# Optimization experiments

Hardware: AMD Instinct MI355X
Metric: run time of the kernel (lower is better)

## Reference

```python
import jax, jax.numpy as jnp
import numpy as np

B, S, H, NH, HD, L, I, M = 2, 2048, 768, 12, 64, 6, 3072, 256
VOCAB, TYPES = 30522, 2
EPS = 1e-6  # layernorm epsilon and FAVOR+ numerical stabilizer


def layer_norm(x, g, b):
    mu = jnp.mean(x, axis=-1, keepdims=True)
    var = jnp.mean(jax.lax.square(x), axis=-1, keepdims=True) - jax.lax.square(mu)
    return (x - mu) * jax.lax.rsqrt(var + EPS) * g + b


def favor_attention(q, k, v, mask, proj):
    # q,k,v: [B,S,NH,HD]; proj: [M,HD] random features; mask: [B,S] float
    dn = 1.0 / np.sqrt(np.sqrt(HD))      # data normalizer for softmax kernel
    ratio = 1.0 / np.sqrt(M)
    qn, kn = q * dn, k * dn
    qp = jnp.einsum('bsnd,md->bsnm', qn, proj)
    kp = jnp.einsum('bsnd,md->bsnm', kn, proj)
    qd = 0.5 * jnp.sum(qn * qn, axis=-1, keepdims=True)
    kd = 0.5 * jnp.sum(kn * kn, axis=-1, keepdims=True)
    # stabilizers: per-position max for queries, global (seq+feature) max for keys
    q_prime = ratio * (jnp.exp(qp - qd - jnp.max(qp, axis=-1, keepdims=True)) + EPS)
    k_prime = ratio * (jnp.exp(kp - kd - jnp.max(kp, axis=(1, 3), keepdims=True)) + EPS)
    k_prime = k_prime * mask[:, :, None, None]
    kv = jnp.einsum('bsnm,bsnd->bnmd', k_prime, v)          # [B,NH,M,HD]
    num = jnp.einsum('bsnm,bnmd->bsnd', q_prime, kv)        # [B,S,NH,HD]
    den = jnp.einsum('bsnm,bnm->bsn', q_prime, jnp.sum(k_prime, axis=1))
    return num / den[..., None]


def setup_inputs() -> dict:
    key = jax.random.key(0)
    ks = jax.random.split(key, 32)
    f = lambda i, shape, s=0.02: (jax.random.normal(ks[i], shape, jnp.float32) * s)
    inp = {
        'input_ids': jax.random.randint(ks[0], (B, S), 0, VOCAB, jnp.int32),
        'token_type_ids': jax.random.randint(ks[1], (B, S), 0, TYPES, jnp.int32),
        'position_ids': jnp.tile(jnp.arange(S, dtype=jnp.int32)[None, :], (B, 1)),
        'attention_mask': jnp.ones((B, S), jnp.int32),
        'word_emb': f(2, (VOCAB, H), 0.1),
        'pos_emb': f(3, (S, H), 0.1),
        'type_emb': f(4, (TYPES, H), 0.1),
        'emb_ln_g': jnp.ones((H,), jnp.float32),
        'emb_ln_b': jnp.zeros((H,), jnp.float32),
        'wq': f(5, (L, H, NH, HD)), 'bq': jnp.zeros((L, NH, HD), jnp.float32),
        'wk': f(6, (L, H, NH, HD)), 'bk': jnp.zeros((L, NH, HD), jnp.float32),
        'wv': f(7, (L, H, NH, HD)), 'bv': jnp.zeros((L, NH, HD), jnp.float32),
        'wo': f(8, (L, NH, HD, H)), 'bo': jnp.zeros((L, H), jnp.float32),
        'ln1_g': jnp.ones((L, H), jnp.float32), 'ln1_b': jnp.zeros((L, H), jnp.float32),
        'wi': f(9, (L, H, I)), 'bi': jnp.zeros((L, I), jnp.float32),
        'wo2': f(10, (L, I, H)), 'bo2': jnp.zeros((L, H), jnp.float32),
        'ln2_g': jnp.ones((L, H), jnp.float32), 'ln2_b': jnp.zeros((L, H), jnp.float32),
        'proj': jax.random.normal(ks[11], (L, M, HD), jnp.float32),
    }
    return inp


def reference(input_ids, token_type_ids, position_ids, attention_mask,
              word_emb, pos_emb, type_emb, emb_ln_g, emb_ln_b,
              wq, bq, wk, bk, wv, bv, wo, bo, ln1_g, ln1_b,
              wi, bi, wo2, bo2, ln2_g, ln2_b, proj):
    mask = attention_mask.astype(jnp.float32)
    x = word_emb[input_ids] + pos_emb[position_ids] + type_emb[token_type_ids]
    x = layer_norm(x, emb_ln_g, emb_ln_b)
    for l in range(L):
        q = jnp.einsum('bsh,hnd->bsnd', x, wq[l]) + bq[l]
        k = jnp.einsum('bsh,hnd->bsnd', x, wk[l]) + bk[l]
        v = jnp.einsum('bsh,hnd->bsnd', x, wv[l]) + bv[l]
        att = favor_attention(q, k, v, mask, proj[l])
        att = jnp.einsum('bsnd,ndh->bsh', att, wo[l]) + bo[l]
        a = layer_norm(att + x, ln1_g[l], ln1_b[l])
        inter = jax.nn.gelu(jnp.einsum('bsh,hi->bsi', a, wi[l]) + bi[l])
        out = jnp.einsum('bsi,ih->bsh', inter, wo2[l]) + bo2[l]
        x = layer_norm(out + a, ln2_g[l], ln2_b[l])
    return x
```

## Files before the change

### kernel.cpp

```cpp
#include <hip/hip_runtime.h>
#include <hip/hip_bf16.h>

#define B_ 2
#define S_ 2048
#define H_ 768
#define NH_ 12
#define HD_ 64
#define L_ 6
#define I_ 3072
#define M_ 256
#define BS_ 4096
#define R_ 49152
#define NXH_ 3145728
#define EPS_ 1e-6f
#define DN_ 0.35355339059327373f
#define RATIO_ 0.0625f

typedef __attribute__((ext_vector_type(8))) short bf16x8;
typedef __attribute__((ext_vector_type(4))) float f32x4;

__device__ __forceinline__ void gload16(const void* g, void* l) {
    __builtin_amdgcn_global_load_lds(
        (const __attribute__((address_space(1))) void*)g,
        (__attribute__((address_space(3))) void*)l, 16, 0, 0);
}

__device__ __forceinline__ float gelu_f(float x) {
    const float c = 0.7978845608028654f;
    float x3 = x * x * x;
    return 0.5f * x * (1.0f + tanhf(c * (x + 0.044715f * x3)));
}

__device__ __forceinline__ unsigned enc_f(float f) {
    unsigned u = __float_as_uint(f);
    return (u & 0x80000000u) ? ~u : (u | 0x80000000u);
}
__device__ __forceinline__ float dec_f(unsigned u) {
    return (u & 0x80000000u) ? __uint_as_float(u & 0x7fffffffu) : __uint_as_float(~u);
}

__device__ __forceinline__ void blockReduceSum2(float& a, float& b) {
    __shared__ float sa[4], sb[4];
    int lane = threadIdx.x & 63, wid = threadIdx.x >> 6;
    #pragma unroll
    for (int off = 32; off; off >>= 1) {
        a += __shfl_down(a, off, 64);
        b += __shfl_down(b, off, 64);
    }
    __syncthreads();
    if (lane == 0) { sa[wid] = a; sb[wid] = b; }
    __syncthreads();
    a = sa[0] + sa[1] + sa[2] + sa[3];
    b = sb[0] + sb[1] + sb[2] + sb[3];
    __syncthreads();
}

template<int ACT, int OUTMODE>
__global__ __launch_bounds__(256) void gemm_pipe3_kernel(
    const __hip_bfloat16* __restrict__ A, const __hip_bfloat16* __restrict__ BT,
    const float* __restrict__ bias, void* __restrict__ Cv,
    int K, int lda, int ldb, int ldc, float* __restrict__ aux)
{
    __shared__ __align__(16) unsigned short As[3][128][32];
    __shared__ __align__(16) unsigned short Bs[3][128][32];
    const int tid = threadIdx.x, lane = tid & 63, wid = tid >> 6;
    const int wr = wid >> 1, wc = wid & 1;
    const size_t r0 = (size_t)blockIdx.y * 128;
    const int n0 = blockIdx.x * 128;
    const size_t kbase = (size_t)blockIdx.z * (size_t)K;

    const int srow = lane >> 2;
    const int selem = ((lane & 3) ^ ((srow >> 1) & 3)) * 8;
    const unsigned short* ga0 = (const unsigned short*)A + (r0 + wid * 32 + srow) * (size_t)lda + kbase + selem;
    const unsigned short* gb0 = (const unsigned short*)BT + ((size_t)n0 + wid * 32 + srow) * (size_t)ldb + kbase + selem;

    f32x4 acc[4][4];
    #pragma unroll
    for (int i = 0; i < 4; i++)
        #pragma unroll
        for (int j = 0; j < 4; j++)
            acc[i][j] = (f32x4){0.f, 0.f, 0.f, 0.f};

    const int lr = lane & 15;
    const int rc8 = (((lane >> 4) ^ ((lr >> 1) & 3))) * 8;

#define STAGE_(t) { const int bb_ = (t) % 3; const int kk_ = (t) * 32;            \
    gload16(ga0 + kk_, &As[bb_][wid * 32][0]);                                    \
    gload16(ga0 + kk_ + 16 * (size_t)lda, &As[bb_][wid * 32 + 16][0]);            \
    gload16(gb0 + kk_, &Bs[bb_][wid * 32][0]);                                    \
    gload16(gb0 + kk_ + 16 * (size_t)ldb, &Bs[bb_][wid * 32 + 16][0]); }

#define ITER_(t, VMSTR, DOSTAGE) {                                                \
    if (DOSTAGE) STAGE_((t) + 2);                                                 \
    asm volatile("s_waitcnt vmcnt(" VMSTR ")" ::: "memory");                      \
    __builtin_amdgcn_sched_barrier(0);                                            \
    __builtin_amdgcn_s_barrier();                                                 \
    __builtin_amdgcn_sched_barrier(0);                                            \
    const int bb_ = (t) % 3;                                                      \
    bf16x8 af[4], bfv[4];                                                         \
    _Pragma("unroll") for (int i = 0; i < 4; i++)                                 \
        af[i] = *(const bf16x8*)&As[bb_][wr * 64 + i * 16 + lr][rc8];             \
    _Pragma("unroll") for (int j = 0; j < 4; j++)                                 \
        bfv[j] = *(const bf16x8*)&Bs[bb_][wc * 64 + j * 16 + lr][rc8];            \
    __builtin_amdgcn_s_setprio(1);                                                \
    _Pragma("unroll") for (int i = 0; i < 4; i++)                                 \
        _Pragma("unroll") for (int j = 0; j < 4; j++)                             \
            acc[i][j] = __builtin_amdgcn_mfma_f32_16x16x32_bf16(af[i], bfv[j], acc[i][j], 0, 0, 0); \
    __builtin_amdgcn_s_setprio(0);                                                \
    __builtin_amdgcn_s_barrier();                                                 \
    __builtin_amdgcn_sched_barrier(0); }

    const int nT = K >> 5;
    STAGE_(0); STAGE_(1);
    for (int t = 0; t < nT - 2; ++t) ITER_(t, "8", true);
    ITER_(nT - 2, "4", false);
    ITER_(nT - 1, "0", false);
#undef ITER_
#undef STAGE_

    const int rr = (lane >> 4) * 4;
    const int cc = lane & 15;
    if (OUTMODE == 3) {
        float* fpl = aux + (size_t)blockIdx.z * NXH_;
        #pragma unroll
        for (int i = 0; i < 4; i++) {
            #pragma unroll
            for (int j = 0; j < 4; j++) {
                size_t col = (size_t)n0 + wc * 64 + j * 16 + cc;
                #pragma unroll
                for (int rg = 0; rg < 4; rg++) {
                    size_t row = r0 + wr * 64 + i * 16 + rr + rg;
                    fpl[row * (size_t)ldc + col] = acc[i][j][rg];
                }
            }
        }
    } else if (OUTMODE == 1) {
        #pragma unroll
        for (int i = 0; i < 4; i++) {
            #pragma unroll
            for (int j = 0; j < 4; j++) {
                size_t col = (size_t)n0 + wc * 64 + j * 16 + cc;
                float bv_ = bias ? bias[col] : 0.f;
                #pragma unroll
                for (int rg = 0; rg < 4; rg++) {
                    size_t row = r0 + wr * 64 + i * 16 + rr + rg;
                    float v = acc[i][j][rg] + bv_;
                    if (ACT == 1) v = gelu_f(v);
                    ((__hip_bfloat16*)Cv)[row * (size_t)ldc + col] = __float2bfloat16(v);
                }
            }
        }
    } else {
        const size_t seg = (size_t)n0 / 768;
        const int colbase = n0 - (int)seg * 768;
        #pragma unroll
        for (int i = 0; i < 4; i++) {
            #pragma unroll
            for (int rg = 0; rg < 4; rg++) {
                size_t row = r0 + wr * 64 + i * 16 + rr + rg;
                float ss = 0.f;
                #pragma unroll
                for (int j = 0; j < 4; j++) {
                    int colw = wc * 64 + j * 16 + cc;
                    size_t col = (size_t)n0 + colw;
                    float bv_ = bias ? bias[col] : 0.f;
                    float v = acc[i][j][rg] + bv_;
                    __hip_bfloat16 hb = __float2bfloat16(v);
                    ((__hip_bfloat16*)Cv)[seg * (size_t)NXH_ + row * 768 + colbase + colw] = hb;
                    float vr = __bfloat162float(hb);
                    ss += vr * vr;
                }
                #pragma unroll
                for (int off = 1; off <= 8; off <<= 1)
                    ss += __shfl_xor(ss, off, 64);
                if (seg < 2 && (lane & 15) == 0) {
                    int nh = colbase / 64 + wc;
                    aux[seg * (size_t)R_ + row * 12 + nh] = 0.5f * DN_ * DN_ * ss;
                }
            }
        }
    }
}

__global__ __launch_bounds__(256) void gemm_pipe3_n64_kernel(
    const __hip_bfloat16* __restrict__ A, const __hip_bfloat16* __restrict__ BT,
    const float* __restrict__ bias, float* __restrict__ C,
    int K, int lda, int ldb, int ldc)
{
    __shared__ __align__(16) unsigned short As[3][128][32];
    __shared__ __align__(16) unsigned short Bs[3][64][32];
    const int tid = threadIdx.x, lane = tid & 63, wid = tid >> 6;
    const size_t r0 = (size_t)blockIdx.y * 128;
    const int n0 = blockIdx.x * 64;

    const int srow = lane >> 2;
    const int selem = ((lane & 3) ^ ((srow >> 1) & 3)) * 8;
    const unsigned short* ga0 = (const unsigned short*)A + (r0 + wid * 32 + srow) * (size_t)lda + selem;
    const unsigned short* gb0 = (const unsigned short*)BT + ((size_t)n0 + wid * 16 + srow) * (size_t)ldb + selem;

    f32x4 acc[2][4];
    #pragma unroll
    for (int i = 0; i < 2; i++)
        #pragma unroll
        for (int j = 0; j < 4; j++)
            acc[i][j] = (f32x4){0.f, 0.f, 0.f, 0.f};

    const int lr = lane & 15;
    const int rc8 = (((lane >> 4) ^ ((lr >> 1) & 3))) * 8;

#define STAGE_(t) { const int bb_ = (t) % 3; const int kk_ = (t) * 32;            \
    gload16(ga0 + kk_, &As[bb_][wid * 32][0]);                                    \
    gload16(ga0 + kk_ + 16 * (size_t)lda, &As[bb_][wid * 32 + 16][0]);            \
    gload16(gb0 + kk_, &Bs[bb_][wid * 16][0]); }

#define ITER_(t, VMSTR, DOSTAGE) {                                                \
    if (DOSTAGE) STAGE_((t) + 2);                                                 \
    asm volatile("s_waitcnt vmcnt(" VMSTR ")" ::: "memory");                      \
    __builtin_amdgcn_sched_barrier(0);                                            \
    __builtin_amdgcn_s_barrier();                                                 \
    __builtin_amdgcn_sched_barrier(0);                                            \
    const int bb_ = (t) % 3;                                                      \
    bf16x8 af[2], bfv[4];                                                         \
    _Pragma("unroll") for (int i = 0; i < 2; i++)                                 \
        af[i] = *(const bf16x8*)&As[bb_][wid * 32 + i * 16 + lr][rc8];            \
    _Pragma("unroll") for (int j = 0; j < 4; j++)                                 \
        bfv[j] = *(const bf16x8*)&Bs[bb_][j * 16 + lr][rc8];                      \
    __builtin_amdgcn_s_setprio(1);                                                \
    _Pragma("unroll") for (int i = 0; i < 2; i++)                                 \
        _Pragma("unroll") for (int j = 0; j < 4; j++)                             \
            acc[i][j] = __builtin_amdgcn_mfma_f32_16x16x32_bf16(af[i], bfv[j], acc[i][j], 0, 0, 0); \
    __builtin_amdgcn_s_setprio(0);                                                \
    __builtin_amdgcn_s_barrier();                                                 \
    __builtin_amdgcn_sched_barrier(0); }

    const int nT = K >> 5;
    STAGE_(0); STAGE_(1);
    for (int t = 0; t < nT - 2; ++t) ITER_(t, "6", true);
    ITER_(nT - 2, "3", false);
    ITER_(nT - 1, "0", false);
#undef ITER_
#undef STAGE_

    const int rr = (lane >> 4) * 4, cc = lane & 15;
    #pragma unroll
    for (int i = 0; i < 2; i++) {
        #pragma unroll
        for (int j = 0; j < 4; j++) {
            int col = n0 + j * 16 + cc;
            float bv_ = bias ? bias[col] : 0.f;
            #pragma unroll
            for (int rg = 0; rg < 4; rg++) {
                size_t row = r0 + wid * 32 + i * 16 + rr + rg;
                C[row * (size_t)ldc + col] = acc[i][j][rg] + bv_;
            }
        }
    }
}

__global__ __launch_bounds__(256) void gemm_projk_kernel(
    const __hip_bfloat16* __restrict__ A, const __hip_bfloat16* __restrict__ BT,
    __hip_bfloat16* __restrict__ Cv,
    int K, int lda, int ldb, int ldc, float alpha,
    unsigned* __restrict__ gmaxu)
{
    __shared__ __align__(16) unsigned short As[2][128][32];
    __shared__ __align__(16) unsigned short Bs[2][128][32];
    __shared__ float rmx[128][2];
    __shared__ float rowm[128];
    const int tid = threadIdx.x, lane = tid & 63, wid = tid >> 6;
    const int wr = wid >> 1, wc = wid & 1;
    const size_t r0 = (size_t)blockIdx.y * 128;
    const int n0 = blockIdx.x * 128;

    const int srow = lane >> 2;
    const int selem = ((lane & 3) ^ ((srow >> 1) & 3)) * 8;
    const unsigned short* ga0 = (const unsigned short*)A + (r0 + wid * 32 + srow) * (size_t)lda + selem;
    const unsigned short* gb0 = (const unsigned short*)BT + ((size_t)n0 + wid * 32 + srow) * (size_t)ldb + selem;

    f32x4 acc[4][4];
    #pragma unroll
    for (int i = 0; i < 4; i++)
        #pragma unroll
        for (int j = 0; j < 4; j++)
            acc[i][j] = (f32x4){0.f, 0.f, 0.f, 0.f};

    gload16(ga0, &As[0][wid * 32][0]);
    gload16(ga0 + 16 * (size_t)lda, &As[0][wid * 32 + 16][0]);
    gload16(gb0, &Bs[0][wid * 32][0]);
    gload16(gb0 + 16 * (size_t)ldb, &Bs[0][wid * 32 + 16][0]);
    __syncthreads();

    const int lr = lane & 15;
    const int rc8 = (((lane >> 4) ^ ((lr >> 1) & 3))) * 8;

    int cur = 0;
    for (int k0 = 0; k0 < K; k0 += 32) {
        const int kn = k0 + 32;
        if (kn < K) {
            gload16(ga0 + kn, &As[cur ^ 1][wid * 32][0]);
            gload16(ga0 + kn + 16 * (size_t)lda, &As[cur ^ 1][wid * 32 + 16][0]);
            gload16(gb0 + kn, &Bs[cur ^ 1][wid * 32][0]);
            gload16(gb0 + kn + 16 * (size_t)ldb, &Bs[cur ^ 1][wid * 32 + 16][0]);
        }
        bf16x8 af[4], bfv[4];
        #pragma unroll
        for (int i = 0; i < 4; i++)
            af[i] = *(const bf16x8*)&As[cur][wr * 64 + i * 16 + lr][rc8];
        #pragma unroll
        for (int j = 0; j < 4; j++)
            bfv[j] = *(const bf16x8*)&Bs[cur][wc * 64 + j * 16 + lr][rc8];
        #pragma unroll
        for (int i = 0; i < 4; i++)
            #pragma unroll
            for (int j = 0; j < 4; j++)
                acc[i][j] = __builtin_amdgcn_mfma_f32_16x16x32_bf16(af[i], bfv[j], acc[i][j], 0, 0, 0);
        __syncthreads();
        cur ^= 1;
    }

    const int rr = (lane >> 4) * 4;
    const int cc = lane & 15;
    #pragma unroll
    for (int i = 0; i < 4; i++) {
        #pragma unroll
        for (int j = 0; j < 4; j++) {
            int colw = wc * 64 + j * 16 + cc;
            size_t col = (size_t)n0 + colw;
            #pragma unroll
            for (int rg = 0; rg < 4; rg++) {
                size_t row = r0 + wr * 64 + i * 16 + rr + rg;
                Cv[row * ldc + col] = __float2bfloat16(acc[i][j][rg] * alpha);
            }
        }
    }
    #pragma unroll
    for (int i = 0; i < 4; i++) {
        #pragma unroll
        for (int rg = 0; rg < 4; rg++) {
            float rm = -3.4e38f;
            #pragma unroll
            for (int j = 0; j < 4; j++) rm = fmaxf(rm, acc[i][j][rg] * alpha);
            #pragma unroll
            for (int off = 1; off <= 8; off <<= 1)
                rm = fmaxf(rm, __shfl_xor(rm, off, 64));
            if ((lane & 15) == 0) rmx[wr * 64 + i * 16 + rr + rg][wc] = rm;
        }
    }
    __syncthreads();
    if (tid < 128) rowm[tid] = fmaxf(rmx[tid][0], rmx[tid][1]);
    __syncthreads();
    if (tid < 12) {
        int b = (int)(r0 / 24576);
        int h = (int)((r0 + tid) % 12);
        float m = -3.4e38f;
        for (int k = tid; k < 128; k += 12) m = fmaxf(m, rowm[k]);
        atomicMax(&gmaxu[b * 12 + h], enc_f(m));
    }
}

__global__ __launch_bounds__(512) void qnum_fused_kernel(
    const __hip_bfloat16* __restrict__ Qbp, const __hip_bfloat16* __restrict__ projb,
    const float* __restrict__ qd, const float* __restrict__ ksum,
    const __hip_bfloat16* __restrict__ kvT, __hip_bfloat16* __restrict__ ATT)
{
    __shared__ __align__(16) unsigned short Pl[128][256];
    __shared__ __align__(16) unsigned short kvTl[64][256];
    __shared__ float ksl[256];
    __shared__ float qdl[128];
    __shared__ float red[128][4];
    __shared__ float rmaxv[128];
    __shared__ float deni[128];
    unsigned short (*Asm)[64] = (unsigned short (*)[64])&Pl[0][0];
    unsigned short (*Bsm)[64] = (unsigned short (*)[64])(&Pl[0][0] + 8192);

    const int tid = threadIdx.x, lane = tid & 63, w = tid >> 6;
    const int wrow = w >> 2, wcol = w & 3;
    const int bn = blockIdx.y, b = bn / NH_, n = bn % NH_;
    const size_t r0g = (size_t)b * S_ + (size_t)blockIdx.x * 128;

    if (tid < 256) ksl[tid] = ksum[(size_t)bn * 256 + tid];
    else if (tid < 384) qdl[tid - 256] = qd[(r0g + tid - 256) * 12 + n];

    const int lrow = lane >> 3, lch = lane & 7;
    const int sch = (lch ^ (lrow & 7)) * 8;
    gload16((const unsigned short*)Qbp + (r0g + w * 16 + lrow) * 768 + n * 64 + sch, &Asm[w * 16][0]);
    gload16((const unsigned short*)Qbp + (r0g + w * 16 + 8 + lrow) * 768 + n * 64 + sch, &Asm[w * 16 + 8][0]);
    #pragma unroll
    for (int p = 0; p < 4; p++)
        gload16((const unsigned short*)projb + (size_t)(w * 32 + p * 8 + lrow) * 64 + sch,
                &Bsm[w * 32 + p * 8][0]);
    {
        const int rIn = lane >> 5, c32 = lane & 31;
        #pragma unroll
        for (int p = 0; p < 4; p++) {
            int d = w * 8 + p * 2 + rIn;
            gload16((const unsigned short*)kvT + (size_t)bn * (HD_ * M_) + (size_t)d * 256
                    + (c32 ^ (d & 7)) * 8, &kvTl[w * 8 + p * 2][0]);
        }
    }
    __syncthreads();

    const int lr = lane & 15, kq = lane >> 4;
    f32x4 acc[4][4];
    #pragma unroll
    for (int i = 0; i < 4; i++)
        #pragma unroll
        for (int j = 0; j < 4; j++)
            acc[i][j] = (f32x4){0.f, 0.f, 0.f, 0.f};

    #pragma unroll
    for (int ks = 0; ks < 2; ks++) {
        const int ch = (((ks << 2) | kq) ^ (lr & 7)) * 8;
        bf16x8 af[4], bfv[4];
        #pragma unroll
        for (int i = 0; i < 4; i++)
            af[i] = *(const bf16x8*)&Asm[wrow * 64 + i * 16 + lr][ch];
        #pragma unroll
        for (int j = 0; j < 4; j++)
            bfv[j] = *(const bf16x8*)&Bsm[wcol * 64 + j * 16 + lr][ch];
        #pragma unroll
        for (int i = 0; i < 4; i++)
            #pragma unroll
            for (int j = 0; j < 4; j++)
                acc[i][j] = __builtin_amdgcn_mfma_f32_16x16x32_bf16(af[i], bfv[j], acc[i][j], 0, 0, 0);
    }

    #pragma unroll
    for (int i = 0; i < 4; i++) {
        #pragma unroll
        for (int rg = 0; rg < 4; rg++) {
            float rm = -3.4e38f;
            #pragma unroll
            for (int j = 0; j < 4; j++) rm = fmaxf(rm, acc[i][j][rg] * DN_);
            #pragma unroll
            for (int off = 1; off <= 8; off <<= 1)
                rm = fmaxf(rm, __shfl_xor(rm, off, 64));
            if ((lane & 15) == 0) red[wrow * 64 + i * 16 + kq * 4 + rg][wcol] = rm;
        }
    }
    __syncthreads();
    if (tid < 128)
        rmaxv[tid] = fmaxf(fmaxf(red[tid][0], red[tid][1]), fmaxf(red[tid][2], red[tid][3]));
    __syncthreads();

    #pragma unroll
    for (int i = 0; i < 4; i++) {
        #pragma unroll
        for (int rg = 0; rg < 4; rg++) {
            int row = wrow * 64 + i * 16 + kq * 4 + rg;
            float qdv = qdl[row], mx = rmaxv[row];
            float dsum = 0.f;
            #pragma unroll
            for (int j = 0; j < 4; j++) {
                int col = wcol * 64 + j * 16 + lr;
                float qp = acc[i][j][rg] * DN_;
                float qv = RATIO_ * (expf(qp - qdv - mx) + EPS_);
                __hip_bfloat16 qb = __float2bfloat16(qv);
                Pl[row][((col >> 3) ^ (row & 7)) * 8 + (col & 7)] = *(unsigned short*)&qb;
                dsum += __bfloat162float(qb) * ksl[col];
            }
            #pragma unroll
            for (int off = 1; off <= 8; off <<= 1)
                dsum += __shfl_xor(dsum, off, 64);
            if ((lane & 15) == 0) red[row][wcol] = dsum;
        }
    }
    __syncthreads();
    if (tid < 128)
        deni[tid] = red[tid][0] + red[tid][1] + red[tid][2] + red[tid][3];
    __syncthreads();

    f32x4 acc2[4];
    #pragma unroll
    for (int j = 0; j < 4; j++) acc2[j] = (f32x4){0.f, 0.f, 0.f, 0.f};
    #pragma unroll
    for (int ks = 0; ks < 8; ks++) {
        const int mc = ks * 4 + kq;
        const int sl = (mc ^ (lr & 7)) * 8;
        bf16x8 af = *(const bf16x8*)&Pl[w * 16 + lr][sl];
        #pragma unroll
        for (int j = 0; j < 4; j++) {
            bf16x8 bfv = *(const bf16x8*)&kvTl[j * 16 + lr][sl];
            acc2[j] = __builtin_amdgcn_mfma_f32_16x16x32_bf16(af, bfv, acc2[j], 0, 0, 0);
        }
    }
    #pragma unroll
    for (int rg = 0; rg < 4; rg++) {
        int row = w * 16 + kq * 4 + rg;
        float inv = 1.0f / deni[row];
        #pragma unroll
        for (int j = 0; j < 4; j++)
            ATT[(r0g + row) * 768 + n * 64 + j * 16 + lr]
                = __float2bfloat16(acc2[j][rg] * inv);
    }
}

__global__ __launch_bounds__(256) void kv_fused_kernel(
    const __hip_bfloat16* __restrict__ KF, const __hip_bfloat16* __restrict__ Vb,
    const float* __restrict__ kd, const unsigned* __restrict__ gmaxu,
    const int* __restrict__ amask,
    float* __restrict__ part, float* __restrict__ kpart)
{
    const int m0 = blockIdx.x * 64, bn = blockIdx.y, b = bn / NH_, n = bn % NH_;
    const int s0 = blockIdx.z * 256;
    __shared__ __align__(16) float As2[16][68];
    __shared__ __align__(16) float Bs2[16][68];
    __shared__ float sred[4][64];
    const int tid = threadIdx.x, tx = tid & 15, ty = tid >> 4;
    const float gm = dec_f(gmaxu[bn]);
    float acc[4][4] = {};
    float ks = 0.f;
    for (int ss = 0; ss < 256; ss += 16) {
        #pragma unroll
        for (int i = 0; i < 4; i++) {
            int idx = tid + i * 256;
            int kk = idx >> 6, c = idx & 63;
            size_t srow = (size_t)b * S_ + s0 + ss + kk;
            float kdv = kd[srow * 12 + n];
            float mk = (float)amask[srow];
            float kf = __bfloat162float(KF[srow * (NH_ * M_) + n * M_ + m0 + c]);
            float kp = RATIO_ * (expf(kf - kdv - gm) + EPS_) * mk;
            As2[kk][c] = kp;
            ks += kp;
            Bs2[kk][c] = __bfloat162float(Vb[srow * H_ + n * HD_ + c]);
        }
        __syncthreads();
        #pragma unroll
        for (int kk = 0; kk < 16; kk++) {
            float4 av = *reinterpret_cast<const float4*>(&As2[kk][ty * 4]);
            float4 bv = *reinterpret_cast<const float4*>(&Bs2[kk][tx * 4]);
            float a4[4] = {av.x, av.y, av.z, av.w};
            float b4[4] = {bv.x, bv.y, bv.z, bv.w};
            #pragma unroll
            for (int i = 0; i < 4; i++)
                #pragma unroll
                for (int j = 0; j < 4; j++)
                    acc[i][j] += a4[i] * b4[j];
        }
        __syncthreads();
    }
    float* Cb = part + ((size_t)blockIdx.z * (B_ * NH_) + bn) * (M_ * HD_);
    #pragma unroll
    for (int j = 0; j < 4; j++)
        #pragma unroll
        for (int i = 0; i < 4; i++)
            Cb[(size_t)(tx * 4 + j) * M_ + m0 + ty * 4 + i] = acc[i][j];
    sred[tid >> 6][tid & 63] = ks;
    __syncthreads();
    if (tid < 64)
        kpart[((size_t)bn * 8 + blockIdx.z) * M_ + m0 + tid]
            = sred[0][tid] + sred[1][tid] + sred[2][tid] + sred[3][tid];
}

__global__ __launch_bounds__(256) void kvred_kernel(
    const float* __restrict__ part, __hip_bfloat16* __restrict__ kvT)
{
    const int bn = blockIdx.x, d = blockIdx.y, m = threadIdx.x;
    float s = 0.f;
    #pragma unroll
    for (int c = 0; c < 8; c++)
        s += part[((size_t)c * (B_ * NH_) + bn) * (M_ * HD_) + (size_t)d * M_ + m];
    kvT[(size_t)bn * (HD_ * M_) + (size_t)d * M_ + m] = __float2bfloat16(s);
}

__global__ __launch_bounds__(256) void prep_kernel(
    const float* __restrict__ wq_l, const float* __restrict__ wk_l,
    const float* __restrict__ wv_l, const float* __restrict__ wo_l,
    const float* __restrict__ wi_l, const float* __restrict__ wo2_l,
    const float* __restrict__ proj_l,
    const float* __restrict__ bq_l, const float* __restrict__ bk_l, const float* __restrict__ bv_l,
    __hip_bfloat16* __restrict__ wqT, __hip_bfloat16* __restrict__ wkT,
    __hip_bfloat16* __restrict__ wvT, __hip_bfloat16* __restrict__ woT,
    __hip_bfloat16* __restrict__ wiT, __hip_bfloat16* __restrict__ wo2T,
    __hip_bfloat16* __restrict__ projb, float* __restrict__ biasq,
    unsigned* __restrict__ gmaxu)
{
    __shared__ float tile[32][33];
    int bid = blockIdx.x;
    if (bid < 6912) {
        const float* src; __hip_bfloat16* dst; int K, N, kt, nt;
        if (bid < 2304) {
            int t = bid / 576, idx = bid % 576;
            src = (t == 0) ? wq_l : (t == 1) ? wk_l : (t == 2) ? wv_l : wo_l;
            dst = (t == 0) ? wqT : (t == 1) ? wkT : (t == 2) ? wvT : woT;
            K = 768; N = 768; kt = idx % 24; nt = idx / 24;
        } else if (bid < 4608) {
            int idx = bid - 2304;
            src = wi_l; dst = wiT; K = 768; N = 3072;
            kt = idx % 24; nt = idx / 24;
        } else {
            int idx = bid - 4608;
            src = wo2_l; dst = wo2T; K = 3072; N = 768;
            kt = idx % 96; nt = idx / 96;
        }
        int k0 = kt * 32, n0 = nt * 32;
        int tx = threadIdx.x & 31, ty = threadIdx.x >> 5;
        #pragma unroll
        for (int i = 0; i < 4; i++)
            tile[ty + i * 8][tx] = src[(size_t)(k0 + ty + i * 8) * N + n0 + tx];
        __syncthreads();
        #pragma unroll
        for (int i = 0; i < 4; i++)
            dst[(size_t)(n0 + ty + i * 8) * K + k0 + tx] = __float2bfloat16(tile[tx][ty + i * 8]);
    } else if (bid < 6976) {
        int i = (bid - 6912) * 256 + threadIdx.x;
        projb[i] = __float2bfloat16(proj_l[i]);
    } else if (bid < 6985) {
        int i = (bid - 6976) * 256 + threadIdx.x;
        if (i < 768) biasq[i] = bq_l[i];
        else if (i < 1536) biasq[i] = bk_l[i - 768];
        else if (i < 2304) biasq[i] = bv_l[i - 1536];
    } else {
        if (threadIdx.x < 24) gmaxu[threadIdx.x] = 0u;
    }
}

__global__ __launch_bounds__(256) void embed_ln_kernel(
    const int* __restrict__ ids, const int* __restrict__ tts, const int* __restrict__ pos,
    const float* __restrict__ wemb, const float* __restrict__ pemb, const float* __restrict__ temb,
    const float* __restrict__ g, const float* __restrict__ bb,
    float* __restrict__ out, __hip_bfloat16* __restrict__ outb)
{
    size_t row = blockIdx.x;
    int id = ids[row], tt = tts[row], ps = pos[row];
    const float* w0 = wemb + (size_t)id * H_;
    const float* p0 = pemb + (size_t)ps * H_;
    const float* t0 = temb + (size_t)tt * H_;
    float vals[3], s1 = 0.f, s2 = 0.f;
    #pragma unroll
    for (int i = 0; i < 3; i++) {
        int h = threadIdx.x + i * 256;
        float v = w0[h] + p0[h] + t0[h];
        vals[i] = v; s1 += v; s2 += v * v;
    }
    blockReduceSum2(s1, s2);
    float mu = s1 * (1.0f / H_);
    float var = s2 * (1.0f / H_) - mu * mu;
    float rs = rsqrtf(var + EPS_);
    #pragma unroll
    for (int i = 0; i < 3; i++) {
        int h = threadIdx.x + i * 256;
        float y = (vals[i] - mu) * rs * g[h] + bb[h];
        out[row * H_ + h] = y;
        outb[row * H_ + h] = __float2bfloat16(y);
    }
}

__global__ __launch_bounds__(256) void add_ln_kernel(
    const float* __restrict__ P, const float* __restrict__ Q,
    const float* __restrict__ g, const float* __restrict__ bb,
    float* __restrict__ out, __hip_bfloat16* __restrict__ outb)
{
    size_t row = blockIdx.x;
    float vals[3], s1 = 0.f, s2 = 0.f;
    #pragma unroll
    for (int i = 0; i < 3; i++) {
        int h = threadIdx.x + i * 256;
        float v = P[row * H_ + h] + Q[row * H_ + h];
        vals[i] = v; s1 += v; s2 += v * v;
    }
    blockReduceSum2(s1, s2);
    float mu = s1 * (1.0f / H_);
    float var = s2 * (1.0f / H_) - mu * mu;
    float rs = rsqrtf(var + EPS_);
    #pragma unroll
    for (int i = 0; i < 3; i++) {
        int h = threadIdx.x + i * 256;
        float y = (vals[i] - mu) * rs * g[h] + bb[h];
        out[row * H_ + h] = y;
        if (outb) outb[row * H_ + h] = __float2bfloat16(y);
    }
}

__global__ __launch_bounds__(256) void add_ln3_kernel(
    const float* __restrict__ planes, const float* __restrict__ bias,
    const float* __restrict__ Q,
    const float* __restrict__ g, const float* __restrict__ bb,
    float* __restrict__ out, __hip_bfloat16* __restrict__ outb)
{
    size_t row = blockIdx.x;
    float vals[3], s1 = 0.f, s2 = 0.f;
    #pragma unroll
    for (int i = 0; i < 3; i++) {
        int h = threadIdx.x + i * 256;
        size_t e = row * H_ + h;
        float v = planes[e] + planes[NXH_ + e] + bias[h] + Q[e];
        vals[i] = v; s1 += v; s2 += v * v;
    }
    blockReduceSum2(s1, s2);
    float mu = s1 * (1.0f / H_);
    float var = s2 * (1.0f / H_) - mu * mu;
    float rs = rsqrtf(var + EPS_);
    #pragma unroll
    for (int i = 0; i < 3; i++) {
        int h = threadIdx.x + i * 256;
        float y = (vals[i] - mu) * rs * g[h] + bb[h];
        out[row * H_ + h] = y;
        outb[row * H_ + h] = __float2bfloat16(y);
    }
}

__global__ __launch_bounds__(256) void ksum_final_kernel(
    const float* __restrict__ part, float* __restrict__ ksum)
{
    int bn = blockIdx.x, m = threadIdx.x;
    float s = 0.f;
    #pragma unroll
    for (int c = 0; c < 8; c++) s += part[((size_t)bn * 8 + c) * M_ + m];
    ksum[(size_t)bn * M_ + m] = s;
}

extern "C" void kernel_launch(void* const* d_in, const int* in_sizes, int n_in,
                              void* d_out, int out_size, void* d_ws, size_t ws_size,
                              hipStream_t stream)
{
    const int* input_ids  = (const int*)d_in[0];
    const int* token_type = (const int*)d_in[1];
    const int* position   = (const int*)d_in[2];
    const int* amask      = (const int*)d_in[3];
    const float* wemb = (const float*)d_in[4];
    const float* pemb = (const float*)d_in[5];
    const float* temb = (const float*)d_in[6];
    const float* elng = (const float*)d_in[7];
    const float* elnb = (const float*)d_in[8];
    const float* wq  = (const float*)d_in[9];
    const float* bq  = (const float*)d_in[10];
    const float* wk  = (const float*)d_in[11];
    const float* bk  = (const float*)d_in[12];
    const float* wv  = (const float*)d_in[13];
    const float* bv  = (const float*)d_in[14];
    const float* wo  = (const float*)d_in[15];
    const float* bo  = (const float*)d_in[16];
    const float* ln1g = (const float*)d_in[17];
    const float* ln1b = (const float*)d_in[18];
    const float* wi  = (const float*)d_in[19];
    const float* bi  = (const float*)d_in[20];
    const float* wo2 = (const float*)d_in[21];
    const float* bo2 = (const float*)d_in[22];
    const float* ln2g = (const float*)d_in[23];
    const float* ln2b = (const float*)d_in[24];
    const float* proj = (const float*)d_in[25];

    float* ws = (float*)d_ws;
    float* X    = ws;
    float* T2   = X + 3145728;
    float* BIG  = T2 + 3145728;
    float* U    = BIG + 12582912;
    __hip_bfloat16* Xb  = (__hip_bfloat16*)(U + 6291456);
    __hip_bfloat16* Qb  = (__hip_bfloat16*)((float*)Xb + 1572864);
    __hip_bfloat16* Kb  = Qb + 3145728;
    __hip_bfloat16* Vb  = Kb + 3145728;
    __hip_bfloat16* BF1 = Vb + 3145728;
    __hip_bfloat16* WT  = BF1 + 3145728;
    float* kvT_f = (float*)(WT + 7094272);
    __hip_bfloat16* kvT = (__hip_bfloat16*)kvT_f;
    float* KSUM  = kvT_f + 196608;
    float* KPART = KSUM + 6144;
    float* RSVD  = KPART + 196608;
    unsigned* GMAXU = (unsigned*)(RSVD + 98304);
    float* QD    = (float*)GMAXU + 64;
    float* KD    = QD + 49152;
    float* BIASQ = KD + 49152;
    float* T1    = (float*)d_out;

    __hip_bfloat16* wqT  = WT;
    __hip_bfloat16* wkT  = wqT + 589824;
    __hip_bfloat16* wvT  = wkT + 589824;
    __hip_bfloat16* woT  = wvT + 589824;
    __hip_bfloat16* wiT  = woT + 589824;
    __hip_bfloat16* wo2T = wiT + 2359296;
    __hip_bfloat16* projb = wo2T + 2359296;
    float* PART = U;
    float* PLANES = U;
    __hip_bfloat16* BIGb = (__hip_bfloat16*)BIG;

    embed_ln_kernel<<<BS_, 256, 0, stream>>>(input_ids, token_type, position,
        wemb, pemb, temb, elng, elnb, X, Xb);

    for (int l = 0; l < L_; l++) {
        const float* wq_l = wq + (size_t)l * H_ * NH_ * HD_;
        const float* wk_l = wk + (size_t)l * H_ * NH_ * HD_;
        const float* wv_l = wv + (size_t)l * H_ * NH_ * HD_;
        const float* wo_l = wo + (size_t)l * NH_ * HD_ * H_;
        const float* bq_l = bq + (size_t)l * NH_ * HD_;
        const float* bk_l = bk + (size_t)l * NH_ * HD_;
        const float* bv_l = bv + (size_t)l * NH_ * HD_;
        const float* bo_l = bo + (size_t)l * H_;
        const float* wi_l = wi + (size_t)l * H_ * I_;
        const float* bi_l = bi + (size_t)l * I_;
        const float* wo2_l = wo2 + (size_t)l * I_ * H_;
        const float* bo2_l = bo2 + (size_t)l * H_;
        const float* proj_l = proj + (size_t)l * M_ * HD_;

        prep_kernel<<<6986, 256, 0, stream>>>(wq_l, wk_l, wv_l, wo_l, wi_l, wo2_l, proj_l,
            bq_l, bk_l, bv_l, wqT, wkT, wvT, woT, wiT, wo2T, projb, BIASQ, GMAXU);

        gemm_pipe3_kernel<0,2><<<dim3(18,32), 256, 0, stream>>>(
            Xb, wqT, BIASQ, (void*)Qb, 768, 768, 768, 768, QD);

        gemm_projk_kernel<<<dim3(2,384), 256, 0, stream>>>(
            Kb, projb, BIGb, 64, 64, 64, 256, DN_, GMAXU);
        kv_fused_kernel<<<dim3(4, B_*NH_, 8), 256, 0, stream>>>(
            BIGb, Vb, KD, GMAXU, amask, PART, KPART);
        ksum_final_kernel<<<B_*NH_, 256, 0, stream>>>(KPART, KSUM);
        kvred_kernel<<<dim3(B_*NH_, HD_), 256, 0, stream>>>(PART, kvT);

        qnum_fused_kernel<<<dim3(16, B_*NH_), 512, 0, stream>>>(
            Qb, projb, QD, KSUM, kvT, BF1);

        gemm_pipe3_n64_kernel<<<dim3(12,32), 256, 0, stream>>>(
            BF1, woT, bo_l, T1, 768, 768, 768, 768);
        add_ln_kernel<<<BS_, 256, 0, stream>>>(T1, X, ln1g + (size_t)l*H_, ln1b + (size_t)l*H_, T2, BF1);

        gemm_pipe3_kernel<1,1><<<dim3(24,32), 256, 0, stream>>>(
            BF1, wiT, bi_l, (void*)BIGb, 768, 768, 768, 3072, nullptr);

        gemm_pipe3_kernel<0,3><<<dim3(6,32,2), 256, 0, stream>>>(
            BIGb, wo2T, nullptr, nullptr, 1536, 3072, 3072, 768, PLANES);
        float* xout = (l == L_ - 1) ? (float*)d_out : X;
        add_ln3_kernel<<<BS_, 256, 0, stream>>>(PLANES, bo2_l, T2,
            ln2g + (size_t)l*H_, ln2b + (size_t)l*H_, xout, Xb);
    }
}
```

Before: 1.631 ms.

## Enlarge GEMM tile to 256x128 and merge ksum reduction into kvred

The pipelined bf16 GEMM now computes a 256x128 output tile per block, with each warp owning 128 rows and 8x4 MFMA accumulators. This raises reuse of each B fragment and halves the block count for the QKV, FFN-up and FFN-down GEMMs. In exchange it uses more registers and LDS, and the grids become smaller (e.g. 192 blocks for FFN-down), which risks underfilling the CUs. The separate ksum_final kernel is also folded into kvred as an extra grid row, removing one launch per layer.

```diff
diff --git a/kernel.cpp b/kernel.cpp
--- a/kernel.cpp
+++ b/kernel.cpp
@@ -56,27 +56,27 @@
 }
 
 template<int ACT, int OUTMODE>
-__global__ __launch_bounds__(256) void gemm_pipe3_kernel(
+__global__ __launch_bounds__(256) void gemm_pipe3w_kernel(
     const __hip_bfloat16* __restrict__ A, const __hip_bfloat16* __restrict__ BT,
     const float* __restrict__ bias, void* __restrict__ Cv,
     int K, int lda, int ldb, int ldc, float* __restrict__ aux)
 {
-    __shared__ __align__(16) unsigned short As[3][128][32];
+    __shared__ __align__(16) unsigned short As[3][256][32];
     __shared__ __align__(16) unsigned short Bs[3][128][32];
     const int tid = threadIdx.x, lane = tid & 63, wid = tid >> 6;
     const int wr = wid >> 1, wc = wid & 1;
-    const size_t r0 = (size_t)blockIdx.y * 128;
+    const size_t r0 = (size_t)blockIdx.y * 256;
     const int n0 = blockIdx.x * 128;
     const size_t kbase = (size_t)blockIdx.z * (size_t)K;
 
     const int srow = lane >> 2;
     const int selem = ((lane & 3) ^ ((srow >> 1) & 3)) * 8;
-    const unsigned short* ga0 = (const unsigned short*)A + (r0 + wid * 32 + srow) * (size_t)lda + kbase + selem;
+    const unsigned short* ga0 = (const unsigned short*)A + (r0 + wid * 64 + srow) * (size_t)lda + kbase + selem;
     const unsigned short* gb0 = (const unsigned short*)BT + ((size_t)n0 + wid * 32 + srow) * (size_t)ldb + kbase + selem;
 
-    f32x4 acc[4][4];
-    #pragma unroll
-    for (int i = 0; i < 4; i++)
+    f32x4 acc[8][4];
+    #pragma unroll
+    for (int i = 0; i < 8; i++)
         #pragma unroll
         for (int j = 0; j < 4; j++)
             acc[i][j] = (f32x4){0.f, 0.f, 0.f, 0.f};
@@ -85,10 +85,12 @@
     const int rc8 = (((lane >> 4) ^ ((lr >> 1) & 3))) * 8;
 
 #define STAGE_(t) { const int bb_ = (t) % 3; const int kk_ = (t) * 32;            \
-    gload16(ga0 + kk_, &As[bb_][wid * 32][0]);                                    \
-    gload16(ga0 + kk_ + 16 * (size_t)lda, &As[bb_][wid * 32 + 16][0]);            \
-    gload16(gb0 + kk_, &Bs[bb_][wid * 32][0]);                                    \
-    gload16(gb0 + kk_ + 16 * (size_t)ldb, &Bs[bb_][wid * 32 + 16][0]); }
+    gload16(ga0 + kk_,                      &As[bb_][wid * 64][0]);               \
+    gload16(ga0 + kk_ + 16 * (size_t)lda,   &As[bb_][wid * 64 + 16][0]);          \
+    gload16(ga0 + kk_ + 32 * (size_t)lda,   &As[bb_][wid * 64 + 32][0]);          \
+    gload16(ga0 + kk_ + 48 * (size_t)lda,   &As[bb_][wid * 64 + 48][0]);          \
+    gload16(gb0 + kk_,                      &Bs[bb_][wid * 32][0]);               \
+    gload16(gb0 + kk_ + 16 * (size_t)ldb,   &Bs[bb_][wid * 32 + 16][0]); }
 
 #define ITER_(t, VMSTR, DOSTAGE) {                                                \
     if (DOSTAGE) STAGE_((t) + 2);                                                 \
@@ -97,23 +99,26 @@
     __builtin_amdgcn_s_barrier();                                                 \
     __builtin_amdgcn_sched_barrier(0);                                            \
     const int bb_ = (t) % 3;                                                      \
-    bf16x8 af[4], bfv[4];                                                         \
-    _Pragma("unroll") for (int i = 0; i < 4; i++)                                 \
-        af[i] = *(const bf16x8*)&As[bb_][wr * 64 + i * 16 + lr][rc8];             \
+    bf16x8 bfv[4];                                                                \
     _Pragma("unroll") for (int j = 0; j < 4; j++)                                 \
         bfv[j] = *(const bf16x8*)&Bs[bb_][wc * 64 + j * 16 + lr][rc8];            \
-    __builtin_amdgcn_s_setprio(1);                                                \
-    _Pragma("unroll") for (int i = 0; i < 4; i++)                                 \
-        _Pragma("unroll") for (int j = 0; j < 4; j++)                             \
-            acc[i][j] = __builtin_amdgcn_mfma_f32_16x16x32_bf16(af[i], bfv[j], acc[i][j], 0, 0, 0); \
-    __builtin_amdgcn_s_setprio(0);                                                \
+    _Pragma("unroll") for (int ih = 0; ih < 2; ih++) {                            \
+        bf16x8 af[4];                                                             \
+        _Pragma("unroll") for (int i = 0; i < 4; i++)                             \
+            af[i] = *(const bf16x8*)&As[bb_][wr * 128 + (ih * 4 + i) * 16 + lr][rc8]; \
+        __builtin_amdgcn_s_setprio(1);                                            \
+        _Pragma("unroll") for (int i = 0; i < 4; i++)                             \
+            _Pragma("unroll") for (int j = 0; j < 4; j++)                         \
+                acc[ih * 4 + i][j] = __builtin_amdgcn_mfma_f32_16x16x32_bf16(af[i], bfv[j], acc[ih * 4 + i][j], 0, 0, 0); \
+        __builtin_amdgcn_s_setprio(0);                                            \
+    }                                                                             \
     __builtin_amdgcn_s_barrier();                                                 \
     __builtin_amdgcn_sched_barrier(0); }
 
     const int nT = K >> 5;
     STAGE_(0); STAGE_(1);
-    for (int t = 0; t < nT - 2; ++t) ITER_(t, "8", true);
-    ITER_(nT - 2, "4", false);
+    for (int t = 0; t < nT - 2; ++t) ITER_(t, "12", true);
+    ITER_(nT - 2, "6", false);
     ITER_(nT - 1, "0", false);
 #undef ITER_
 #undef STAGE_
@@ -123,27 +128,27 @@
     if (OUTMODE == 3) {
         float* fpl = aux + (size_t)blockIdx.z * NXH_;
         #pragma unroll
-        for (int i = 0; i < 4; i++) {
+        for (int i = 0; i < 8; i++) {
             #pragma unroll
             for (int j = 0; j < 4; j++) {
                 size_t col = (size_t)n0 + wc * 64 + j * 16 + cc;
                 #pragma unroll
                 for (int rg = 0; rg < 4; rg++) {
-                    size_t row = r0 + wr * 64 + i * 16 + rr + rg;
+                    size_t row = r0 + wr * 128 + i * 16 + rr + rg;
                     fpl[row * (size_t)ldc + col] = acc[i][j][rg];
                 }
             }
         }
     } else if (OUTMODE == 1) {
         #pragma unroll
-        for (int i = 0; i < 4; i++) {
+        for (int i = 0; i < 8; i++) {
             #pragma unroll
             for (int j = 0; j < 4; j++) {
                 size_t col = (size_t)n0 + wc * 64 + j * 16 + cc;
                 float bv_ = bias ? bias[col] : 0.f;
                 #pragma unroll
                 for (int rg = 0; rg < 4; rg++) {
-                    size_t row = r0 + wr * 64 + i * 16 + rr + rg;
+                    size_t row = r0 + wr * 128 + i * 16 + rr + rg;
                     float v = acc[i][j][rg] + bv_;
                     if (ACT == 1) v = gelu_f(v);
                     ((__hip_bfloat16*)Cv)[row * (size_t)ldc + col] = __float2bfloat16(v);
@@ -154,10 +159,10 @@
         const size_t seg = (size_t)n0 / 768;
         const int colbase = n0 - (int)seg * 768;
         #pragma unroll
-        for (int i = 0; i < 4; i++) {
+        for (int i = 0; i < 8; i++) {
             #pragma unroll
             for (int rg = 0; rg < 4; rg++) {
-                size_t row = r0 + wr * 64 + i * 16 + rr + rg;
+                size_t row = r0 + wr * 128 + i * 16 + rr + rg;
                 float ss = 0.f;
                 #pragma unroll
                 for (int j = 0; j < 4; j++) {
@@ -553,14 +558,22 @@
 }
 
 __global__ __launch_bounds__(256) void kvred_kernel(
-    const float* __restrict__ part, __hip_bfloat16* __restrict__ kvT)
+    const float* __restrict__ part, __hip_bfloat16* __restrict__ kvT,
+    const float* __restrict__ kpart, float* __restrict__ ksum)
 {
     const int bn = blockIdx.x, d = blockIdx.y, m = threadIdx.x;
-    float s = 0.f;
-    #pragma unroll
-    for (int c = 0; c < 8; c++)
-        s += part[((size_t)c * (B_ * NH_) + bn) * (M_ * HD_) + (size_t)d * M_ + m];
-    kvT[(size_t)bn * (HD_ * M_) + (size_t)d * M_ + m] = __float2bfloat16(s);
+    if (d < 64) {
+        float s = 0.f;
+        #pragma unroll
+        for (int c = 0; c < 8; c++)
+            s += part[((size_t)c * (B_ * NH_) + bn) * (M_ * HD_) + (size_t)d * M_ + m];
+        kvT[(size_t)bn * (HD_ * M_) + (size_t)d * M_ + m] = __float2bfloat16(s);
+    } else {
+        float s = 0.f;
+        #pragma unroll
+        for (int c = 0; c < 8; c++) s += kpart[((size_t)bn * 8 + c) * M_ + m];
+        ksum[(size_t)bn * M_ + m] = s;
+    }
 }
 
 __global__ __launch_bounds__(256) void prep_kernel(
@@ -698,16 +711,6 @@
         out[row * H_ + h] = y;
         outb[row * H_ + h] = __float2bfloat16(y);
     }
-}
-
-__global__ __launch_bounds__(256) void ksum_final_kernel(
-    const float* __restrict__ part, float* __restrict__ ksum)
-{
-    int bn = blockIdx.x, m = threadIdx.x;
-    float s = 0.f;
-    #pragma unroll
-    for (int c = 0; c < 8; c++) s += part[((size_t)bn * 8 + c) * M_ + m];
-    ksum[(size_t)bn * M_ + m] = s;
 }
 
 extern "C" void kernel_launch(void* const* d_in, const int* in_sizes, int n_in,
@@ -795,15 +798,14 @@
         prep_kernel<<<6986, 256, 0, stream>>>(wq_l, wk_l, wv_l, wo_l, wi_l, wo2_l, proj_l,
             bq_l, bk_l, bv_l, wqT, wkT, wvT, woT, wiT, wo2T, projb, BIASQ, GMAXU);
 
-        gemm_pipe3_kernel<0,2><<<dim3(18,32), 256, 0, stream>>>(
+        gemm_pipe3w_kernel<0,2><<<dim3(18,16), 256, 0, stream>>>(
             Xb, wqT, BIASQ, (void*)Qb, 768, 768, 768, 768, QD);
 
         gemm_projk_kernel<<<dim3(2,384), 256, 0, stream>>>(
             Kb, projb, BIGb, 64, 64, 64, 256, DN_, GMAXU);
         kv_fused_kernel<<<dim3(4, B_*NH_, 8), 256, 0, stream>>>(
             BIGb, Vb, KD, GMAXU, amask, PART, KPART);
-        ksum_final_kernel<<<B_*NH_, 256, 0, stream>>>(KPART, KSUM);
-        kvred_kernel<<<dim3(B_*NH_, HD_), 256, 0, stream>>>(PART, kvT);
+        kvred_kernel<<<dim3(B_*NH_, HD_+1), 256, 0, stream>>>(PART, kvT, KPART, KSUM);
 
         qnum_fused_kernel<<<dim3(16, B_*NH_), 512, 0, stream>>>(
             Qb, projb, QD, KSUM, kvT, BF1);
@@ -812,10 +814,10 @@
             BF1, woT, bo_l, T1, 768, 768, 768, 768);
         add_ln_kernel<<<BS_, 256, 0, stream>>>(T1, X, ln1g + (size_t)l*H_, ln1b + (size_t)l*H_, T2, BF1);
 
-        gemm_pipe3_kernel<1,1><<<dim3(24,32), 256, 0, stream>>>(
+        gemm_pipe3w_kernel<1,1><<<dim3(24,16), 256, 0, stream>>>(
             BF1, wiT, bi_l, (void*)BIGb, 768, 768, 768, 3072, nullptr);
 
-        gemm_pipe3_kernel<0,3><<<dim3(6,32,2), 256, 0, stream>>>(
+        gemm_pipe3w_kernel<0,3><<<dim3(6,16,2), 256, 0, stream>>>(
             BIGb, wo2T, nullptr, nullptr, 1536, 3072, 3072, 768, PLANES);
         float* xout = (l == L_ - 1) ? (float*)d_out : X;
         add_ln3_kernel<<<BS_, 256, 0, stream>>>(PLANES, bo2_l, T2,
```

New measurement: 2.313 ms. +41.8%, slower.
